# Kernel tuning notes

Hardware: AMD Instinct MI355X
Metric: run time of the kernel (lower is better)

## Reference

```python
import jax, jax.numpy as jnp
import numpy as np

E, NH, G = 2048, 16, 4
HD = E // NH          # head_dim = 128
KV = E // G           # kv proj width = 512 == G * HD
B, S = 2, 2048


def setup_inputs() -> dict:
    key = jax.random.key(0)
    ks = jax.random.split(key, 7)
    s = lambda n: 1.0 / np.sqrt(n)
    return {
        "query": jax.random.normal(ks[0], (B, S, E), jnp.float32),
        "key_in": jax.random.normal(ks[1], (B, S, E), jnp.float32),
        "value": jax.random.normal(ks[2], (B, S, E), jnp.float32),
        "Wq": jax.random.normal(ks[3], (E, E), jnp.float32) * s(E),
        "bq": jnp.zeros((E,), jnp.float32),
        "Wk": jax.random.normal(ks[4], (E, KV), jnp.float32) * s(E),
        "bk": jnp.zeros((KV,), jnp.float32),
        "Wv": jax.random.normal(ks[5], (E, KV), jnp.float32) * s(E),
        "bv": jnp.zeros((KV,), jnp.float32),
        "Wo": jax.random.normal(ks[6], (E, E), jnp.float32) * s(E),
        "bo": jnp.zeros((E,), jnp.float32),
    }


def reference(query, key_in, value, Wq, bq, Wk, bk, Wv, bv, Wo, bo):
    b, s, _ = query.shape
    scale = HD ** -0.5
    # projections
    q = (query @ Wq + bq).reshape(b, s, NH, HD).transpose(0, 2, 1, 3)   # [B,NH,S,HD]
    k = (key_in @ Wk + bk).reshape(b, s, G, HD).transpose(0, 2, 1, 3)   # [B,G,S,HD]
    v = (value @ Wv + bv).reshape(b, s, G, HD).transpose(0, 2, 1, 3)    # [B,G,S,HD]
    # grouped-query attention: each KV head serves NH//G query heads
    qg = q.reshape(b, G, NH // G, s, HD)                                # [B,G,NH/G,S,HD]
    scores = jnp.einsum('bgqsh,bgth->bgqst', qg, k) * scale             # [B,G,NH/G,S,S]
    w = jax.nn.softmax(scores, axis=-1)
    out = jnp.einsum('bgqst,bgth->bgqsh', w, v)                         # [B,G,NH/G,S,HD]
    out = out.reshape(b, NH, s, HD).transpose(0, 2, 1, 3).reshape(b, s, E)
    return out @ Wo + bo
```

## Files before the change

### kernel.cpp

```cpp
#include <hip/hip_runtime.h>
#include <hip/hip_bf16.h>

#define E_ 2048
#define S_ 2048
#define B_ 2
#define BS_ 4096
#define KV_ 512
#define NH_ 16
#define G_ 4
#define HD_ 128
#define QK_SCALE 0.08838834764831845f
#define LOG2E_ 1.4426950408889634f

typedef __attribute__((ext_vector_type(8))) short short8;
typedef __attribute__((ext_vector_type(4))) float floatx4;
typedef __attribute__((ext_vector_type(4))) unsigned short ushort4_;

static __device__ __forceinline__ unsigned short f2bf(float f) {
  unsigned int u = __builtin_bit_cast(unsigned int, f);
  u += 0x7fffu + ((u >> 16) & 1u);
  return (unsigned short)(u >> 16);
}

static __device__ __forceinline__ unsigned int cvt_pk_bf16(float lo, float hi) {
  unsigned int r;
  asm("v_cvt_pk_bf16_f32 %0, %1, %2" : "=v"(r) : "v"(lo), "v"(hi));
  return r;
}

static __device__ __forceinline__ void gld16(const void* g, void* l) {
  __builtin_amdgcn_global_load_lds(
      (const __attribute__((address_space(1))) unsigned int*)g,
      (__attribute__((address_space(3))) unsigned int*)l, 16, 0, 0);
}

__global__ __launch_bounds__(256) void k_prep(
    const float* __restrict__ Wq, unsigned short* __restrict__ WqT,
    const float* __restrict__ Wk, unsigned short* __restrict__ WkT,
    const float* __restrict__ Wv, unsigned short* __restrict__ WvT,
    const float* __restrict__ Wo, unsigned short* __restrict__ WoT) {
  __shared__ float ts[32][33];
  int t = blockIdx.x;
  const float* in; unsigned short* out; int N; int rem;
  if (t < 4096)      { in = Wq; out = WqT; N = 2048; rem = t; }
  else if (t < 5120) { in = Wk; out = WkT; N = 512;  rem = t - 4096; }
  else if (t < 6144) { in = Wv; out = WvT; N = 512;  rem = t - 5120; }
  else               { in = Wo; out = WoT; N = 2048; rem = t - 6144; }
  const int K = 2048;
  int nx = N >> 5;
  int bx = rem % nx, by = rem / nx;
  int tx = threadIdx.x & 31, ty = threadIdx.x >> 5;
  int n0 = bx * 32, k0 = by * 32;
#pragma unroll
  for (int i = 0; i < 4; ++i)
    ts[ty + i * 8][tx] = in[(size_t)(k0 + ty + i * 8) * N + n0 + tx];
  __syncthreads();
#pragma unroll
  for (int i = 0; i < 4; ++i)
    out[(size_t)(n0 + ty + i * 8) * K + k0 + tx] = f2bf(ts[tx][ty + i * 8]);
}

template <bool OUT_F32, bool A_F32, bool B_F32>
static __device__ __forceinline__ void gemm_bt_tile(
    const void* __restrict__ A, const void* __restrict__ Bt,
    const float* __restrict__ bias, bool rowBias, void* __restrict__ C,
    int N, int K, float scale, int bx, int by,
    unsigned short* As, unsigned short* Bs) {
  const int tid = threadIdx.x;
  const int w = tid >> 6;
  const int lhi = (tid >> 4) & 3;
  const int llo = tid & 15;
  const int wr = w >> 1, wc = w & 1;
  const size_t brow = (size_t)by * 128, bcol = (size_t)bx * 128;

  auto stage = [&](int k0, int bufi) {
#pragma unroll
    for (int i = 0; i < 2; ++i) {
      int o = i * 256 + tid;
      if constexpr (A_F32) {
        int row = o >> 2, gcol = o & 3;
        const float4* src = reinterpret_cast<const float4*>(
            (const float*)A + (brow + row) * (size_t)K + k0 + gcol * 8);
        float4 v0 = src[0], v1 = src[1];
        uint4 pk = {cvt_pk_bf16(v0.x, v0.y), cvt_pk_bf16(v0.z, v0.w),
                    cvt_pk_bf16(v1.x, v1.y), cvt_pk_bf16(v1.z, v1.w)};
        *reinterpret_cast<uint4*>(As + bufi * 4096 + (size_t)o * 8) = pk;
      } else {
        gld16((const unsigned short*)A + (brow + (o >> 2)) * (size_t)K + k0 + (o & 3) * 8,
              As + bufi * 4096 + (size_t)(i * 256 + w * 64) * 8);
      }
      if constexpr (B_F32) {
        int row = o >> 2, gcol = o & 3;
        const float4* src = reinterpret_cast<const float4*>(
            (const float*)Bt + (bcol + row) * (size_t)K + k0 + gcol * 8);
        float4 v0 = src[0], v1 = src[1];
        uint4 pk = {cvt_pk_bf16(v0.x, v0.y), cvt_pk_bf16(v0.z, v0.w),
                    cvt_pk_bf16(v1.x, v1.y), cvt_pk_bf16(v1.z, v1.w)};
        *reinterpret_cast<uint4*>(Bs + bufi * 4096 + (size_t)o * 8) = pk;
      } else {
        gld16((const unsigned short*)Bt + (bcol + (o >> 2)) * (size_t)K + k0 + (o & 3) * 8,
              Bs + bufi * 4096 + (size_t)(i * 256 + w * 64) * 8);
      }
    }
  };

  floatx4 acc[4][4];
#pragma unroll
  for (int i = 0; i < 4; ++i)
#pragma unroll
    for (int j = 0; j < 4; ++j)
      acc[i][j] = (floatx4){0.f, 0.f, 0.f, 0.f};

  stage(0, 0);
  __syncthreads();
  int buf = 0;
  const int nk = K >> 5;
  for (int t = 0; t < nk; ++t) {
    if (t + 1 < nk) stage((t + 1) * 32, buf ^ 1);
    const unsigned short* Ab = As + buf * 4096;
    const unsigned short* Bb = Bs + buf * 4096;
    short8 a[4], b[4];
#pragma unroll
    for (int f = 0; f < 4; ++f) {
      a[f] = *reinterpret_cast<const short8*>(Ab + (wr * 64 + f * 16 + llo) * 32 + lhi * 8);
      b[f] = *reinterpret_cast<const short8*>(Bb + (wc * 64 + f * 16 + llo) * 32 + lhi * 8);
    }
    __builtin_amdgcn_s_setprio(1);
#pragma unroll
    for (int i = 0; i < 4; ++i)
#pragma unroll
      for (int j = 0; j < 4; ++j)
        acc[i][j] = __builtin_amdgcn_mfma_f32_16x16x32_bf16(a[i], b[j], acc[i][j], 0, 0, 0);
    __builtin_amdgcn_s_setprio(0);
    __syncthreads();
    buf ^= 1;
  }

#pragma unroll
  for (int i = 0; i < 4; ++i) {
#pragma unroll
    for (int j = 0; j < 4; ++j) {
      size_t gr0 = brow + wr * 64 + i * 16 + lhi * 4;
      size_t gc = bcol + wc * 64 + j * 16 + llo;
#pragma unroll
      for (int r = 0; r < 4; ++r) {
        size_t grow = gr0 + r;
        float v = acc[i][j][r];
        v += rowBias ? bias[grow] : bias[gc];
        v *= scale;
        if (OUT_F32)
          ((float*)C)[grow * N + gc] = v;
        else
          ((unsigned short*)C)[grow * N + gc] = f2bf(v);
      }
    }
  }
}

__global__ __launch_bounds__(256) void k_gemm_qkv(
    const float* __restrict__ query, const unsigned short* __restrict__ WqT,
    const float* __restrict__ bq, unsigned short* __restrict__ qb,
    const float* __restrict__ key_in, const unsigned short* __restrict__ WkT,
    const float* __restrict__ bk, unsigned short* __restrict__ kb,
    const unsigned short* __restrict__ WvT, const float* __restrict__ value,
    const float* __restrict__ bv, unsigned short* __restrict__ vtb) {
  __shared__ __align__(16) unsigned short As[2 * 128 * 32];
  __shared__ __align__(16) unsigned short Bs[2 * 128 * 32];
  int bid = blockIdx.x;
  if (bid < 512) {
    int xcd = bid & 7, u = bid >> 3;
    int by = (xcd >> 1) * 8 + (u & 7);
    int bx = (xcd & 1) * 8 + (u >> 3);
    gemm_bt_tile<false, true, false>(query, WqT, bq, false, qb, E_, E_,
                                     QK_SCALE * LOG2E_, bx, by, As, Bs);
  } else if (bid < 640) {
    int u = bid - 512;
    int cm = (u & 7) * 16 + (u >> 3);
    gemm_bt_tile<false, true, false>(key_in, WkT, bk, false, kb, KV_, E_, 1.0f,
                                     cm >> 5, cm & 31, As, Bs);
  } else {
    int u = bid - 640;
    int cm = (u & 7) * 16 + (u >> 3);
    gemm_bt_tile<false, false, true>(WvT, value, bv, true, vtb, BS_, E_, 1.0f,
                                     cm >> 2, cm & 3, As, Bs);
  }
}

__global__ __launch_bounds__(256) void k_gemm_o(
    const unsigned short* __restrict__ A, const unsigned short* __restrict__ Bt,
    const float* __restrict__ bias, float* __restrict__ C) {
  __shared__ __align__(16) unsigned short As[2 * 128 * 32];
  __shared__ __align__(16) unsigned short Bs[2 * 128 * 32];
  int xcd = blockIdx.x & 7, u = blockIdx.x >> 3;
  int by = (xcd >> 1) * 8 + (u & 7);
  int bx = (xcd & 1) * 8 + (u >> 3);
  gemm_bt_tile<true, false, false>(A, Bt, bias, false, C, E_, E_, 1.0f,
                                   bx, by, As, Bs);
}

__global__ __launch_bounds__(512) void k_attn(
    const unsigned short* __restrict__ qb, const unsigned short* __restrict__ kb,
    const unsigned short* __restrict__ vt, unsigned short* __restrict__ attn) {
  __shared__ __align__(16) unsigned short Ks[2][64 * 128];
  __shared__ __align__(16) unsigned short Vs[2][128 * 64];
  __shared__ __align__(16) unsigned short Ps[8][32 * 64];

  const int tid = threadIdx.x;
  const int w = tid >> 6;
  const int lhi = (tid >> 4) & 3;
  const int llo = tid & 15;
  const int bid = blockIdx.x;
  const int xcd = bid & 7;
  const int b = xcd >> 2, g = xcd & 3;
  const int inner = bid >> 3;
  const int hq = inner & 3, qt = inner >> 2;
  const int h = g * 4 + hq;

  char* PsW = (char*)&Ps[0][0] + w * 4096;

  short8 qf[2][4];
#pragma unroll
  for (int rt = 0; rt < 2; ++rt)
#pragma unroll
    for (int hc = 0; hc < 4; ++hc) {
      int row = qt * 256 + w * 32 + rt * 16 + llo;
      qf[rt][hc] = *reinterpret_cast<const short8*>(
          qb + ((size_t)(b * 2048 + row)) * 2048 + h * 128 + hc * 32 + lhi * 8);
    }

  floatx4 acc[2][8];
#pragma unroll
  for (int rt = 0; rt < 2; ++rt)
#pragma unroll
    for (int dc = 0; dc < 8; ++dc)
      acc[rt][dc] = (floatx4){0.f, 0.f, 0.f, 0.f};
  float m_[2] = {-1e30f, -1e30f};
  float l_[2] = {0.f, 0.f};

  auto stage = [&](int kv0, int buf) {
#pragma unroll
    for (int i = 0; i < 2; ++i) {
      int o = i * 512 + tid;
      int row = o >> 4, gr2 = (o & 15) ^ (row & 7);
      gld16(kb + ((size_t)(b * 2048 + kv0 + row)) * 512 + g * 128 + gr2 * 8,
            &Ks[buf][(size_t)(i * 512 + w * 64) * 8]);
    }
#pragma unroll
    for (int i = 0; i < 2; ++i) {
      int o = i * 512 + tid;
      int row = o >> 3, gr2 = (o & 7) ^ (row & 7);
      gld16(vt + ((size_t)(g * 128 + row)) * 4096 + b * 2048 + kv0 + gr2 * 8,
            &Vs[buf][(size_t)(i * 512 + w * 64) * 8]);
    }
  };

  stage(0, 0);
  __syncthreads();
  int buf = 0;

  for (int t = 0; t < 32; ++t) {
    const int kv0 = t * 64;
    if (t < 31) stage(kv0 + 64, buf ^ 1);

    floatx4 sc[2][4];
#pragma unroll
    for (int rt = 0; rt < 2; ++rt)
#pragma unroll
      for (int c = 0; c < 4; ++c)
        sc[rt][c] = (floatx4){0.f, 0.f, 0.f, 0.f};
    __builtin_amdgcn_s_setprio(1);
#pragma unroll
    for (int c = 0; c < 4; ++c) {
      int krow = c * 16 + llo;
#pragma unroll
      for (int hc = 0; hc < 4; ++hc) {
        int byteoff = krow * 256 + ((hc * 64 + lhi * 16) ^ ((krow & 7) << 4));
        short8 kf = *reinterpret_cast<const short8*>((const char*)&Ks[buf][0] + byteoff);
        sc[0][c] = __builtin_amdgcn_mfma_f32_16x16x32_bf16(kf, qf[0][hc], sc[0][c], 0, 0, 0);
        sc[1][c] = __builtin_amdgcn_mfma_f32_16x16x32_bf16(kf, qf[1][hc], sc[1][c], 0, 0, 0);
      }
    }
    __builtin_amdgcn_s_setprio(0);

#pragma unroll
    for (int rt = 0; rt < 2; ++rt) {
      float pm = sc[rt][0][0];
#pragma unroll
      for (int c = 0; c < 4; ++c)
#pragma unroll
        for (int r = 0; r < 4; ++r) pm = fmaxf(pm, sc[rt][c][r]);
      if (__any(pm > m_[rt] + 8.0f)) {
        float t2 = pm;
        t2 = fmaxf(t2, __shfl_xor(t2, 16));
        t2 = fmaxf(t2, __shfl_xor(t2, 32));
        float m2 = fmaxf(m_[rt], t2);
        float scr = __builtin_amdgcn_exp2f(m_[rt] - m2);
        m_[rt] = m2;
        l_[rt] *= scr;
#pragma unroll
        for (int r = 0; r < 4; ++r) {
          float s_r = __shfl(scr, (tid & 48) | (((tid >> 2) & 12) + r));
#pragma unroll
          for (int dc = 0; dc < 8; ++dc) acc[rt][dc][r] *= s_r;
        }
      }
      float lsum = l_[rt];
#pragma unroll
      for (int c = 0; c < 4; ++c) {
        float e0 = __builtin_amdgcn_exp2f(sc[rt][c][0] - m_[rt]);
        float e1 = __builtin_amdgcn_exp2f(sc[rt][c][1] - m_[rt]);
        float e2 = __builtin_amdgcn_exp2f(sc[rt][c][2] - m_[rt]);
        float e3 = __builtin_amdgcn_exp2f(sc[rt][c][3] - m_[rt]);
        lsum += (e0 + e1) + (e2 + e3);
        uint2 pk;
        pk.x = cvt_pk_bf16(e0, e1);
        pk.y = cvt_pk_bf16(e2, e3);
        int byteoff = (rt * 16 + llo) * 128 + ((c * 32 + lhi * 8) ^ ((llo & 7) << 4));
        *reinterpret_cast<uint2*>(PsW + byteoff) = pk;
      }
      l_[rt] = lsum;
    }

    short8 pf[2][2];
#pragma unroll
    for (int rt = 0; rt < 2; ++rt)
#pragma unroll
      for (int kc = 0; kc < 2; ++kc) {
        int byteoff = (rt * 16 + llo) * 128 + ((kc * 64 + lhi * 16) ^ ((llo & 7) << 4));
        pf[rt][kc] = *reinterpret_cast<const short8*>(PsW + byteoff);
      }
    __builtin_amdgcn_s_setprio(1);
#pragma unroll
    for (int dc = 0; dc < 8; ++dc) {
      int vrow = dc * 16 + llo;
      int bo0 = vrow * 128 + ((lhi * 16) ^ ((vrow & 7) << 4));
      int bo1 = vrow * 128 + ((64 + lhi * 16) ^ ((vrow & 7) << 4));
      short8 vf0 = *reinterpret_cast<const short8*>((const char*)&Vs[buf][0] + bo0);
      short8 vf1 = *reinterpret_cast<const short8*>((const char*)&Vs[buf][0] + bo1);
      acc[0][dc] = __builtin_amdgcn_mfma_f32_16x16x32_bf16(pf[0][0], vf0, acc[0][dc], 0, 0, 0);
      acc[1][dc] = __builtin_amdgcn_mfma_f32_16x16x32_bf16(pf[1][0], vf0, acc[1][dc], 0, 0, 0);
      acc[0][dc] = __builtin_amdgcn_mfma_f32_16x16x32_bf16(pf[0][1], vf1, acc[0][dc], 0, 0, 0);
      acc[1][dc] = __builtin_amdgcn_mfma_f32_16x16x32_bf16(pf[1][1], vf1, acc[1][dc], 0, 0, 0);
    }
    __builtin_amdgcn_s_setprio(0);
    __syncthreads();
    buf ^= 1;
  }

#pragma unroll
  for (int rt = 0; rt < 2; ++rt) {
    float t2 = l_[rt];
    t2 += __shfl_xor(t2, 16);
    t2 += __shfl_xor(t2, 32);
    float linv = 1.0f / t2;
    float lr[4];
#pragma unroll
    for (int r = 0; r < 4; ++r)
      lr[r] = __shfl(linv, (tid & 48) | (((tid >> 2) & 12) + r));
#pragma unroll
    for (int dc = 0; dc < 8; ++dc)
#pragma unroll
      for (int r = 0; r < 4; ++r) {
        int row = qt * 256 + w * 32 + rt * 16 + lhi * 4 + r;
        float v = acc[rt][dc][r] * lr[r];
        attn[((size_t)(b * 2048 + row)) * 2048 + h * 128 + dc * 16 + llo] = f2bf(v);
      }
  }
}

extern "C" void kernel_launch(void* const* d_in, const int* in_sizes, int n_in,
                              void* d_out, int out_size, void* d_ws, size_t ws_size,
                              hipStream_t stream) {
  const float* query  = (const float*)d_in[0];
  const float* key_in = (const float*)d_in[1];
  const float* value  = (const float*)d_in[2];
  const float* Wq = (const float*)d_in[3];
  const float* bq = (const float*)d_in[4];
  const float* Wk = (const float*)d_in[5];
  const float* bk = (const float*)d_in[6];
  const float* Wv = (const float*)d_in[7];
  const float* bv = (const float*)d_in[8];
  const float* Wo = (const float*)d_in[9];
  const float* bo = (const float*)d_in[10];
  float* out = (float*)d_out;

  char* ws = (char*)d_ws;
  size_t off = 0;
  auto alloc = [&](size_t bytes) {
    char* p = ws + off;
    off += (bytes + 255) & ~(size_t)255;
    return p;
  };
  unsigned short* WqT  = (unsigned short*)alloc((size_t)E_ * E_ * 2);
  unsigned short* WkT  = (unsigned short*)alloc((size_t)KV_ * E_ * 2);
  unsigned short* WvT  = (unsigned short*)alloc((size_t)KV_ * E_ * 2);
  unsigned short* WoT  = (unsigned short*)alloc((size_t)E_ * E_ * 2);
  unsigned short* qb   = (unsigned short*)alloc((size_t)BS_ * E_ * 2);
  unsigned short* kb   = (unsigned short*)alloc((size_t)BS_ * KV_ * 2);
  unsigned short* vtb  = (unsigned short*)alloc((size_t)KV_ * BS_ * 2);
  unsigned short* attb = (unsigned short*)alloc((size_t)BS_ * E_ * 2);

  k_prep<<<10240, 256, 0, stream>>>(Wq, WqT, Wk, WkT, Wv, WvT, Wo, WoT);
  k_gemm_qkv<<<768, 256, 0, stream>>>(query, WqT, bq, qb, key_in, WkT, bk, kb,
                                      WvT, value, bv, vtb);
  k_attn<<<B_ * NH_ * (S_ / 256), 512, 0, stream>>>(qb, kb, vtb, attb);
  k_gemm_o<<<512, 256, 0, stream>>>(attb, WoT, bo, out);
}
```

Before: 232.8 us.

## Stage fp32 GEMM operands via async global-to-LDS loads and convert on fragment read

For the fp32-input GEMM operands (query, key_in, value), the raw fp32 tiles are now copied straight into LDS with the async global-to-LDS path, using an XOR swizzle. The bf16 conversion moves to fragment-load time instead of going through registers during staging. The aim is to overlap global loads with MFMA work as the bf16 path already does, at the cost of double the LDS footprint for those operands and repeated conversion work per fragment read. It also changes the block-to-tile mapping of the output-projection GEMM for a different XCD/L2 locality pattern.

```diff
diff --git a/kernel.cpp b/kernel.cpp
--- a/kernel.cpp
+++ b/kernel.cpp
@@ -72,36 +72,52 @@
   const int llo = tid & 15;
   const int wr = w >> 1, wc = w & 1;
   const size_t brow = (size_t)by * 128, bcol = (size_t)bx * 128;
+  constexpr int ASTR = A_F32 ? 8192 : 4096;
+  constexpr int BSTR = B_F32 ? 8192 : 4096;
 
   auto stage = [&](int k0, int bufi) {
-#pragma unroll
-    for (int i = 0; i < 2; ++i) {
-      int o = i * 256 + tid;
-      if constexpr (A_F32) {
-        int row = o >> 2, gcol = o & 3;
-        const float4* src = reinterpret_cast<const float4*>(
-            (const float*)A + (brow + row) * (size_t)K + k0 + gcol * 8);
-        float4 v0 = src[0], v1 = src[1];
-        uint4 pk = {cvt_pk_bf16(v0.x, v0.y), cvt_pk_bf16(v0.z, v0.w),
-                    cvt_pk_bf16(v1.x, v1.y), cvt_pk_bf16(v1.z, v1.w)};
-        *reinterpret_cast<uint4*>(As + bufi * 4096 + (size_t)o * 8) = pk;
-      } else {
+    if constexpr (A_F32) {
+#pragma unroll
+      for (int i = 0; i < 4; ++i) {
+        int o = i * 256 + tid;
+        int row = o >> 3, gs = (o & 7) ^ (row & 7);
+        gld16((const float*)A + (brow + row) * (size_t)K + k0 + gs * 4,
+              As + bufi * ASTR + (size_t)(i * 256 + w * 64) * 8);
+      }
+    } else {
+#pragma unroll
+      for (int i = 0; i < 2; ++i) {
+        int o = i * 256 + tid;
         gld16((const unsigned short*)A + (brow + (o >> 2)) * (size_t)K + k0 + (o & 3) * 8,
-              As + bufi * 4096 + (size_t)(i * 256 + w * 64) * 8);
-      }
-      if constexpr (B_F32) {
-        int row = o >> 2, gcol = o & 3;
-        const float4* src = reinterpret_cast<const float4*>(
-            (const float*)Bt + (bcol + row) * (size_t)K + k0 + gcol * 8);
-        float4 v0 = src[0], v1 = src[1];
-        uint4 pk = {cvt_pk_bf16(v0.x, v0.y), cvt_pk_bf16(v0.z, v0.w),
-                    cvt_pk_bf16(v1.x, v1.y), cvt_pk_bf16(v1.z, v1.w)};
-        *reinterpret_cast<uint4*>(Bs + bufi * 4096 + (size_t)o * 8) = pk;
-      } else {
+              As + bufi * ASTR + (size_t)(i * 256 + w * 64) * 8);
+      }
+    }
+    if constexpr (B_F32) {
+#pragma unroll
+      for (int i = 0; i < 4; ++i) {
+        int o = i * 256 + tid;
+        int row = o >> 3, gs = (o & 7) ^ (row & 7);
+        gld16((const float*)Bt + (bcol + row) * (size_t)K + k0 + gs * 4,
+              Bs + bufi * BSTR + (size_t)(i * 256 + w * 64) * 8);
+      }
+    } else {
+#pragma unroll
+      for (int i = 0; i < 2; ++i) {
+        int o = i * 256 + tid;
         gld16((const unsigned short*)Bt + (bcol + (o >> 2)) * (size_t)K + k0 + (o & 3) * 8,
-              Bs + bufi * 4096 + (size_t)(i * 256 + w * 64) * 8);
-      }
-    }
+              Bs + bufi * BSTR + (size_t)(i * 256 + w * 64) * 8);
+      }
+    }
+  };
+
+  auto frag_f32 = [&](const unsigned short* buf, int row) -> short8 {
+    const char* p = (const char*)buf;
+    int g0 = (lhi * 2) ^ (row & 7);
+    float4 v0 = *reinterpret_cast<const float4*>(p + row * 128 + g0 * 16);
+    float4 v1 = *reinterpret_cast<const float4*>(p + row * 128 + (g0 ^ 1) * 16);
+    uint4 pk = {cvt_pk_bf16(v0.x, v0.y), cvt_pk_bf16(v0.z, v0.w),
+                cvt_pk_bf16(v1.x, v1.y), cvt_pk_bf16(v1.z, v1.w)};
+    return __builtin_bit_cast(short8, pk);
   };
 
   floatx4 acc[4][4];
@@ -117,13 +133,21 @@
   const int nk = K >> 5;
   for (int t = 0; t < nk; ++t) {
     if (t + 1 < nk) stage((t + 1) * 32, buf ^ 1);
-    const unsigned short* Ab = As + buf * 4096;
-    const unsigned short* Bb = Bs + buf * 4096;
+    const unsigned short* Ab = As + buf * ASTR;
+    const unsigned short* Bb = Bs + buf * BSTR;
     short8 a[4], b[4];
 #pragma unroll
     for (int f = 0; f < 4; ++f) {
-      a[f] = *reinterpret_cast<const short8*>(Ab + (wr * 64 + f * 16 + llo) * 32 + lhi * 8);
-      b[f] = *reinterpret_cast<const short8*>(Bb + (wc * 64 + f * 16 + llo) * 32 + lhi * 8);
+      int ra = wr * 64 + f * 16 + llo;
+      int rb = wc * 64 + f * 16 + llo;
+      if constexpr (A_F32)
+        a[f] = frag_f32(Ab, ra);
+      else
+        a[f] = *reinterpret_cast<const short8*>(Ab + ra * 32 + lhi * 8);
+      if constexpr (B_F32)
+        b[f] = frag_f32(Bb, rb);
+      else
+        b[f] = *reinterpret_cast<const short8*>(Bb + rb * 32 + lhi * 8);
     }
     __builtin_amdgcn_s_setprio(1);
 #pragma unroll
@@ -164,25 +188,25 @@
     const float* __restrict__ bk, unsigned short* __restrict__ kb,
     const unsigned short* __restrict__ WvT, const float* __restrict__ value,
     const float* __restrict__ bv, unsigned short* __restrict__ vtb) {
-  __shared__ __align__(16) unsigned short As[2 * 128 * 32];
-  __shared__ __align__(16) unsigned short Bs[2 * 128 * 32];
+  __shared__ __align__(16) unsigned short lds[24576];
   int bid = blockIdx.x;
   if (bid < 512) {
     int xcd = bid & 7, u = bid >> 3;
     int by = (xcd >> 1) * 8 + (u & 7);
     int bx = (xcd & 1) * 8 + (u >> 3);
     gemm_bt_tile<false, true, false>(query, WqT, bq, false, qb, E_, E_,
-                                     QK_SCALE * LOG2E_, bx, by, As, Bs);
+                                     QK_SCALE * LOG2E_, bx, by,
+                                     lds, lds + 16384);
   } else if (bid < 640) {
     int u = bid - 512;
     int cm = (u & 7) * 16 + (u >> 3);
     gemm_bt_tile<false, true, false>(key_in, WkT, bk, false, kb, KV_, E_, 1.0f,
-                                     cm >> 5, cm & 31, As, Bs);
+                                     cm >> 5, cm & 31, lds, lds + 16384);
   } else {
     int u = bid - 640;
     int cm = (u & 7) * 16 + (u >> 3);
     gemm_bt_tile<false, false, true>(WvT, value, bv, true, vtb, BS_, E_, 1.0f,
-                                     cm >> 2, cm & 3, As, Bs);
+                                     cm >> 2, cm & 3, lds, lds + 8192);
   }
 }
 
@@ -191,11 +215,9 @@
     const float* __restrict__ bias, float* __restrict__ C) {
   __shared__ __align__(16) unsigned short As[2 * 128 * 32];
   __shared__ __align__(16) unsigned short Bs[2 * 128 * 32];
-  int xcd = blockIdx.x & 7, u = blockIdx.x >> 3;
-  int by = (xcd >> 1) * 8 + (u & 7);
-  int bx = (xcd & 1) * 8 + (u >> 3);
+  int cm = (blockIdx.x & 7) * 64 + (blockIdx.x >> 3);
   gemm_bt_tile<true, false, false>(A, Bt, bias, false, C, E_, E_, 1.0f,
-                                   bx, by, As, Bs);
+                                   cm >> 5, cm & 31, As, Bs);
 }
 
 __global__ __launch_bounds__(512) void k_attn(
```

Result: no change. 228.6 us (-1.8%).
